# Performance work log

Hardware: AMD Instinct MI355X
Metric: run time of the kernel (lower is better)

Reference implementation:

```python
import jax, jax.numpy as jnp
import numpy as np

B, F, O, DEG = 8192, 512, 512, 15  # degree+1 = 16 basis terms


def setup_inputs() -> dict:
    key = jax.random.key(0)
    k1, k2, k3 = jax.random.split(key, 3)
    x = jax.random.normal(k1, (B, F), dtype=jnp.float32)
    coeffs = jax.random.normal(k2, (F, O, DEG + 1), dtype=jnp.float32) * 0.05
    base_weight = jax.random.normal(k3, (F, O), dtype=jnp.float32) * 0.05
    return {"x": x, "coeffs": coeffs, "base_weight": base_weight}


def _chebyshev_basis(x, degree):
    # x: [B, F] -> basis: [B, F, degree+1], vectorized across all features.
    t = jnp.tanh(x)
    T0 = jnp.ones_like(t)
    T1 = t
    basis = [T0, T1]
    for _ in range(2, degree + 1):
        basis.append(2.0 * t * basis[-1] - basis[-2])
    return jnp.stack(basis, axis=-1)  # [B, F, D+1]


def reference(x, coeffs, base_weight):
    basis = _chebyshev_basis(x, DEG)                      # [B, F, D+1]
    poly_out = jnp.einsum('bin,ion->bo', basis, coeffs)   # [B, O]
    kl = jnp.zeros((1,), dtype=x.dtype)
    residual = x @ base_weight                            # [B, O]
    return (poly_out + residual, kl)
```

## Files before the change

kernel.cpp:

```cpp
#include <hip/hip_runtime.h>
#include <hip/hip_bf16.h>
#include <stdint.h>

#define MB_ 8192
#define FD  512
#define OD  512
#define KD  8704
#define KBASIS 8192
#define BT_KS   1088
#define BT_CHUNKS_PER_CT (BT_KS * 128)
#define BT_BYTES_PER_CT  (BT_CHUNKS_PER_CT * 16)
#define TOFF 65536
#define WS_T    16777216ull
#define WS_XBF  8388608ull
#define WS_BT2  8912896ull
#define WS_P1_OFF (WS_T + WS_XBF + WS_BT2)
#define WS_NEED   (WS_P1_OFF + 16777216ull)

typedef __attribute__((ext_vector_type(4))) float f32x4;
typedef __attribute__((ext_vector_type(8))) short bf16x8;
typedef __attribute__((ext_vector_type(4))) unsigned int u32x4;
typedef __attribute__((ext_vector_type(2))) unsigned int u32x2;

__device__ __forceinline__ void gload_lds16(const void* g, void* l) {
  __builtin_amdgcn_global_load_lds((const __attribute__((address_space(1))) void*)g,
                                   (__attribute__((address_space(3))) void*)l,
                                   16, 0, 0);
}

__device__ __forceinline__ uint32_t bf_rtn(float f) {
  uint32_t u = __float_as_uint(f);
  return (u + 0x7fffu + ((u >> 16) & 1u)) >> 16;
}

__device__ __forceinline__ uint32_t pk(float a, float b) {
  uint32_t r;
  asm("v_cvt_pk_bf16_f32 %0, %1, %2" : "=v"(r) : "v"(a), "v"(b));
  return r;
}

__global__ __launch_bounds__(256) void k_tanh(const float* __restrict__ x,
                                              float* __restrict__ t,
                                              uint16_t* __restrict__ xbf) {
  int i = blockIdx.x * 256 + threadIdx.x;
  f32x4 v = ((const f32x4*)x)[i];
  f32x4 tv;
  tv[0] = tanhf(v[0]); tv[1] = tanhf(v[1]);
  tv[2] = tanhf(v[2]); tv[3] = tanhf(v[3]);
  ((f32x4*)t)[i] = tv;
  u32x2 p;
  p[0] = pk(v[0], v[1]);
  p[1] = pk(v[2], v[3]);
  ((u32x2*)xbf)[i] = p;
}

__global__ __launch_bounds__(256) void k_bt(const float* __restrict__ coeffs,
                                            const float* __restrict__ bw,
                                            uint16_t* __restrict__ bt2,
                                            float* __restrict__ out) {
  int tid = blockIdx.x * 256 + threadIdx.x;
  {
    int o = tid & 511, i = tid >> 9;
    const f32x4* src = (const f32x4*)(coeffs + (((size_t)(i * 512 + o)) << 4));
    f32x4 c0 = src[0], c1 = src[1], c2 = src[2], c3 = src[3];
    u32x4 qa, qb;
    qa[0] = pk(c0[0], c0[1]);
    qa[1] = pk(c0[2], c0[3]);
    qa[2] = pk(c1[0], c1[1]);
    qa[3] = pk(c1[2], c1[3]);
    qb[0] = pk(c2[0], c2[1]);
    qb[1] = pk(c2[2], c2[3]);
    qb[2] = pk(c3[0], c3[1]);
    qb[3] = pk(c3[2], c3[3]);
    int slo = ((i >> 2) << 3) | (i & 3);
    size_t cidx = (size_t)(o >> 7) * BT_CHUNKS_PER_CT + (size_t)slo * 128 + (o & 127);
    u32x4* base = (u32x4*)bt2;
    base[cidx]       = qa;
    base[cidx + 512] = qb;
  }
  {
    int o2 = tid >> 9, i2 = tid & 511;
    size_t cidx = (size_t)(o2 >> 7) * BT_CHUNKS_PER_CT + (size_t)(1024 + (i2 >> 3)) * 128 + (o2 & 127);
    bt2[cidx * 8 + (i2 & 7)] = (uint16_t)bf_rtn(bw[i2 * 512 + o2]);
  }
  if (tid == 0) out[(size_t)MB_ * OD] = 0.0f;
}

template <int MODE>
__device__ __forceinline__ void gemm_body(int bx, char* lds,
                                          const float* __restrict__ t,
                                          const uint16_t* __restrict__ xbf,
                                          const uint16_t* __restrict__ bt2,
                                          float* __restrict__ outp) {
  constexpr int S0 = (MODE == 2) ? 68 : 0;

  const int tid  = threadIdx.x;
  const int lane = tid & 63;
  const int wid  = tid >> 6;
  const int wr   = wid >> 1;
  const int wc   = wid & 1;
  const int l15  = lane & 15, l4 = lane >> 4;

  int idx = bx >> 3;
  int rt  = (bx & 7) * 8 + (idx >> 2);
  int ct  = idx & 3;
  const int brow = rt << 7, bcol = ct << 7;

  const char* btbase = (const char*)bt2 + (size_t)ct * BT_BYTES_PER_CT;
  const int row = brow + wr * 32 + l15;
  const uint16_t* x0 = xbf + (size_t)row * FD;
  const uint16_t* x1 = x0 + (size_t)16 * FD;

  const char* bb0 = lds + l4 * 2048 + (wc * 64 + l15) * 16;
  const char* tb0 = lds + TOFF + (wr * 32 + l15) * 16 + l4 * 4;
  char* sBl = lds + tid * 16;
  char* sTl = lds + TOFF + wid * 1024 + lane * 16;

  const char* sBgBase = btbase + (size_t)tid * 16;
  const char* sTgBase = (const char*)t + (((size_t)(brow + wid * 64 + lane)) * FD) * 4;

  f32x4 acc[2][4];
#pragma unroll
  for (int m = 0; m < 2; ++m)
#pragma unroll
    for (int n = 0; n < 4; ++n) acc[m][n] = (f32x4)0.0f;

  u32x4 pf00 = {}, pf01 = {}, pf10 = {}, pf11 = {};

  auto stageB = [&](int gs, int b2) {
    const char* src = sBgBase + ((size_t)gs << 14);
    gload_lds16(src, sBl + b2 * 16384);
    gload_lds16(src + 8192, sBl + b2 * 16384 + 8192);
  };
  auto stageT = [&](int gs, int b2) {
    if (wid < 2)
      gload_lds16(sTgBase + ((size_t)gs << 4), sTl + b2 * 2048);
  };
  auto chains = [&](const char* tb, u32x4& af00, u32x4& af01,
                    u32x4& af10, u32x4& af11) {
#pragma unroll
    for (int m = 0; m < 2; ++m) {
      float tv = *(const float*)(tb + m * 256);
      float c2 = tv + tv;
      float T0 = 1.0f, T1 = tv;
      float T2  = __builtin_fmaf(c2, T1,  -T0);
      float T3  = __builtin_fmaf(c2, T2,  -T1);
      float T4  = __builtin_fmaf(c2, T3,  -T2);
      float T5  = __builtin_fmaf(c2, T4,  -T3);
      float T6  = __builtin_fmaf(c2, T5,  -T4);
      float T7  = __builtin_fmaf(c2, T6,  -T5);
      float T8  = __builtin_fmaf(c2, T7,  -T6);
      float T9  = __builtin_fmaf(c2, T8,  -T7);
      float T10 = __builtin_fmaf(c2, T9,  -T8);
      float T11 = __builtin_fmaf(c2, T10, -T9);
      float T12 = __builtin_fmaf(c2, T11, -T10);
      float T13 = __builtin_fmaf(c2, T12, -T11);
      float T14 = __builtin_fmaf(c2, T13, -T12);
      float T15 = __builtin_fmaf(c2, T14, -T13);
      u32x4 lo, hi;
      lo[0] = pk(T0,  T1);  lo[1] = pk(T2,  T3);
      lo[2] = pk(T4,  T5);  lo[3] = pk(T6,  T7);
      hi[0] = pk(T8,  T9);  hi[1] = pk(T10, T11);
      hi[2] = pk(T12, T13); hi[3] = pk(T14, T15);
      if (m == 0) { af00 = lo; af01 = hi; }
      else        { af10 = lo; af11 = hi; }
    }
  };
  auto mfma16 = [&](const char* bb, const u32x4& af00, const u32x4& af01,
                    const u32x4& af10, const u32x4& af11) {
    bf16x8 a00 = *(const bf16x8*)&af00;
    bf16x8 a01 = *(const bf16x8*)&af01;
    bf16x8 a10 = *(const bf16x8*)&af10;
    bf16x8 a11 = *(const bf16x8*)&af11;
#pragma unroll
    for (int n = 0; n < 4; ++n) {
      bf16x8 b0 = *(const bf16x8*)(bb + n * 256);
      bf16x8 b1 = *(const bf16x8*)(bb + 8192 + n * 256);
      acc[0][n] = __builtin_amdgcn_mfma_f32_16x16x32_bf16(a00, b0, acc[0][n], 0, 0, 0);
      acc[1][n] = __builtin_amdgcn_mfma_f32_16x16x32_bf16(a10, b0, acc[1][n], 0, 0, 0);
      acc[0][n] = __builtin_amdgcn_mfma_f32_16x16x32_bf16(a01, b1, acc[0][n], 0, 0, 0);
      acc[1][n] = __builtin_amdgcn_mfma_f32_16x16x32_bf16(a11, b1, acc[1][n], 0, 0, 0);
    }
  };
  auto fence_bar = [&]() {
    if (wid < 2) asm volatile("s_waitcnt vmcnt(6)" ::: "memory");
    else         asm volatile("s_waitcnt vmcnt(4)" ::: "memory");
    __builtin_amdgcn_s_barrier();
    __builtin_amdgcn_sched_barrier(0);
  };
  auto pairbody = [&](int s, int c0, int c1) {
    u32x4 af00, af01, af10, af11;
    chains(tb0 + c0 * 2048, af00, af01, af10, af11);
    __builtin_amdgcn_s_setprio(1);
    mfma16(bb0 + c0 * 16384, af00, af01, af10, af11);
    __builtin_amdgcn_s_setprio(0);
    chains(tb0 + c1 * 2048, af00, af01, af10, af11);
    __builtin_amdgcn_s_setprio(1);
    mfma16(bb0 + c1 * 16384, af00, af01, af10, af11);
    __builtin_amdgcn_s_setprio(0);
    __builtin_amdgcn_s_barrier();
    __builtin_amdgcn_sched_barrier(0);
    stageB(S0 + s + 4, c0); stageT(S0 + s + 4, c0);
    stageB(S0 + s + 5, c1); stageT(S0 + s + 5, c1);
    fence_bar();
  };

  stageB(S0 + 0, 0); stageT(S0 + 0, 0);
  stageB(S0 + 1, 1); stageT(S0 + 1, 1);
  stageB(S0 + 2, 2); stageT(S0 + 2, 2);
  stageB(S0 + 3, 3); stageT(S0 + 3, 3);
  fence_bar();

  if constexpr (MODE == 0) {
    for (int s = 0; s < 120; s += 4) { pairbody(s, 0, 1); pairbody(s + 2, 2, 3); }
    pairbody(120, 0, 1); pairbody(122, 2, 3);
    for (int s = 124; s < 136; ++s) {
      u32x4 af00 = pf00, af01 = pf01, af10 = pf10, af11 = pf11;
      if (s >= 126 && s <= 133) stageB(s + 2, (s + 2) & 3);
      if (s >= 127 && s <= 134) {
        int kres = ((s + 1 - 128) << 6) + l4 * 8;
        pf00 = *(const u32x4*)(x0 + kres);
        pf01 = *(const u32x4*)(x0 + kres + 32);
        pf10 = *(const u32x4*)(x1 + kres);
        pf11 = *(const u32x4*)(x1 + kres + 32);
      }
      if (s < 128) chains(tb0 + (s & 3) * 2048, af00, af01, af10, af11);
      mfma16(bb0 + (s & 3) * 16384, af00, af01, af10, af11);
      __syncthreads();
    }
  } else if constexpr (MODE == 1) {
    for (int s = 0; s < 64; s += 4) { pairbody(s, 0, 1); pairbody(s + 2, 2, 3); }
    for (int s = 64; s < 68; ++s) {
      u32x4 af00, af01, af10, af11;
      chains(tb0 + (s & 3) * 2048, af00, af01, af10, af11);
      mfma16(bb0 + (s & 3) * 16384, af00, af01, af10, af11);
      __syncthreads();
    }
  } else {
    for (int s = 0; s < 56; s += 4) { pairbody(s, 0, 1); pairbody(s + 2, 2, 3); }
    for (int s = 56; s < 68; ++s) {
      u32x4 af00 = pf00, af01 = pf01, af10 = pf10, af11 = pf11;
      if (s >= 58 && s <= 65) stageB(68 + s + 2, (s + 2) & 3);
      if (s >= 59 && s <= 66) {
        int kres = ((s + 1 - 60) << 6) + l4 * 8;
        pf00 = *(const u32x4*)(x0 + kres);
        pf01 = *(const u32x4*)(x0 + kres + 32);
        pf10 = *(const u32x4*)(x1 + kres);
        pf11 = *(const u32x4*)(x1 + kres + 32);
      }
      if (s < 60) chains(tb0 + (s & 3) * 2048, af00, af01, af10, af11);
      mfma16(bb0 + (s & 3) * 16384, af00, af01, af10, af11);
      __syncthreads();
    }
  }

#pragma unroll
  for (int m = 0; m < 2; ++m)
#pragma unroll
    for (int n = 0; n < 4; ++n)
#pragma unroll
      for (int r = 0; r < 4; ++r) {
        int grow = brow + wr * 32 + m * 16 + l4 * 4 + r;
        int gcol = bcol + wc * 64 + n * 16 + l15;
        outp[(size_t)grow * OD + gcol] = acc[m][n][r];
      }
}

__global__ __launch_bounds__(512, 4) void k_gemm_split(const float* __restrict__ t,
                                                       const uint16_t* __restrict__ xbf,
                                                       const uint16_t* __restrict__ bt2,
                                                       float* __restrict__ out,
                                                       float* __restrict__ p1) {
  __shared__ __align__(128) char lds[73728];
  if (blockIdx.x < 256) gemm_body<1>(blockIdx.x,       lds, t, xbf, bt2, out);
  else                  gemm_body<2>(blockIdx.x - 256, lds, t, xbf, bt2, p1);
}

__global__ __launch_bounds__(512, 2) void k_gemm_full(const float* __restrict__ t,
                                                      const uint16_t* __restrict__ xbf,
                                                      const uint16_t* __restrict__ bt2,
                                                      float* __restrict__ out) {
  __shared__ __align__(128) char lds[73728];
  gemm_body<0>(blockIdx.x, lds, t, xbf, bt2, out);
}

__global__ __launch_bounds__(256) void k_add(float* __restrict__ out,
                                             const float* __restrict__ p1) {
  size_t i = (size_t)blockIdx.x * 256 + threadIdx.x;
  f32x4 a = ((const f32x4*)out)[i];
  f32x4 b = ((const f32x4*)p1)[i];
  a[0] += b[0]; a[1] += b[1]; a[2] += b[2]; a[3] += b[3];
  ((f32x4*)out)[i] = a;
}

extern "C" void kernel_launch(void* const* d_in, const int* in_sizes, int n_in,
                              void* d_out, int out_size, void* d_ws, size_t ws_size,
                              hipStream_t stream) {
  const float* x      = (const float*)d_in[0];
  const float* coeffs = (const float*)d_in[1];
  const float* bw     = (const float*)d_in[2];
  float* out = (float*)d_out;
  char* ws = (char*)d_ws;

  float*    t   = (float*)ws;
  uint16_t* xbf = (uint16_t*)(ws + WS_T);
  uint16_t* bt2 = (uint16_t*)(ws + WS_T + WS_XBF);
  float*    p1  = (float*)(ws + WS_P1_OFF);

  k_tanh<<<4096, 256, 0, stream>>>(x, t, xbf);
  k_bt<<<1024, 256, 0, stream>>>(coeffs, bw, bt2, out);
  if (ws_size >= WS_NEED) {
    k_gemm_split<<<512, 512, 0, stream>>>(t, xbf, bt2, out, p1);
    k_add<<<4096, 256, 0, stream>>>(out, p1);
  } else {
    k_gemm_full<<<256, 512, 0, stream>>>(t, xbf, bt2, out);
  }
}
```

Measured before the change: 104.2 us.

## Replace split-K partial buffer and add kernel with atomic accumulation; merge prep kernels

Both split-K halves of the GEMM now atomically add their fp32 results into a zeroed output. This removes the separate partial buffer, the extra add kernel and its 32 MB of traffic. The tanh/bf16 conversion and the coefficient repacking kernels are merged into one launch, and the non-split fallback path is deleted. In exchange it adds a memset of the output plus atomic read-modify-write stores, and the summation order of the two halves is no longer fixed.

```diff
diff --git a/kernel.cpp b/kernel.cpp
--- a/kernel.cpp
+++ b/kernel.cpp
@@ -13,9 +13,6 @@
 #define TOFF 65536
 #define WS_T    16777216ull
 #define WS_XBF  8388608ull
-#define WS_BT2  8912896ull
-#define WS_P1_OFF (WS_T + WS_XBF + WS_BT2)
-#define WS_NEED   (WS_P1_OFF + 16777216ull)
 
 typedef __attribute__((ext_vector_type(4))) float f32x4;
 typedef __attribute__((ext_vector_type(8))) short bf16x8;
@@ -39,51 +36,50 @@
   return r;
 }
 
-__global__ __launch_bounds__(256) void k_tanh(const float* __restrict__ x,
+__global__ __launch_bounds__(256) void k_prep(const float* __restrict__ x,
                                               float* __restrict__ t,
-                                              uint16_t* __restrict__ xbf) {
-  int i = blockIdx.x * 256 + threadIdx.x;
-  f32x4 v = ((const f32x4*)x)[i];
-  f32x4 tv;
-  tv[0] = tanhf(v[0]); tv[1] = tanhf(v[1]);
-  tv[2] = tanhf(v[2]); tv[3] = tanhf(v[3]);
-  ((f32x4*)t)[i] = tv;
-  u32x2 p;
-  p[0] = pk(v[0], v[1]);
-  p[1] = pk(v[2], v[3]);
-  ((u32x2*)xbf)[i] = p;
-}
-
-__global__ __launch_bounds__(256) void k_bt(const float* __restrict__ coeffs,
-                                            const float* __restrict__ bw,
-                                            uint16_t* __restrict__ bt2,
-                                            float* __restrict__ out) {
-  int tid = blockIdx.x * 256 + threadIdx.x;
-  {
-    int o = tid & 511, i = tid >> 9;
-    const f32x4* src = (const f32x4*)(coeffs + (((size_t)(i * 512 + o)) << 4));
-    f32x4 c0 = src[0], c1 = src[1], c2 = src[2], c3 = src[3];
-    u32x4 qa, qb;
-    qa[0] = pk(c0[0], c0[1]);
-    qa[1] = pk(c0[2], c0[3]);
-    qa[2] = pk(c1[0], c1[1]);
-    qa[3] = pk(c1[2], c1[3]);
-    qb[0] = pk(c2[0], c2[1]);
-    qb[1] = pk(c2[2], c2[3]);
-    qb[2] = pk(c3[0], c3[1]);
-    qb[3] = pk(c3[2], c3[3]);
-    int slo = ((i >> 2) << 3) | (i & 3);
-    size_t cidx = (size_t)(o >> 7) * BT_CHUNKS_PER_CT + (size_t)slo * 128 + (o & 127);
-    u32x4* base = (u32x4*)bt2;
-    base[cidx]       = qa;
-    base[cidx + 512] = qb;
+                                              uint16_t* __restrict__ xbf,
+                                              const float* __restrict__ coeffs,
+                                              const float* __restrict__ bw,
+                                              uint16_t* __restrict__ bt2) {
+  if (blockIdx.x < 4096) {
+    int i = blockIdx.x * 256 + threadIdx.x;
+    f32x4 v = ((const f32x4*)x)[i];
+    f32x4 tv;
+    tv[0] = tanhf(v[0]); tv[1] = tanhf(v[1]);
+    tv[2] = tanhf(v[2]); tv[3] = tanhf(v[3]);
+    ((f32x4*)t)[i] = tv;
+    u32x2 p;
+    p[0] = pk(v[0], v[1]);
+    p[1] = pk(v[2], v[3]);
+    ((u32x2*)xbf)[i] = p;
+  } else {
+    int tid = (blockIdx.x - 4096) * 256 + threadIdx.x;
+    {
+      int o = tid & 511, i = tid >> 9;
+      const f32x4* src = (const f32x4*)(coeffs + (((size_t)(i * 512 + o)) << 4));
+      f32x4 c0 = src[0], c1 = src[1], c2 = src[2], c3 = src[3];
+      u32x4 qa, qb;
+      qa[0] = pk(c0[0], c0[1]);
+      qa[1] = pk(c0[2], c0[3]);
+      qa[2] = pk(c1[0], c1[1]);
+      qa[3] = pk(c1[2], c1[3]);
+      qb[0] = pk(c2[0], c2[1]);
+      qb[1] = pk(c2[2], c2[3]);
+      qb[2] = pk(c3[0], c3[1]);
+      qb[3] = pk(c3[2], c3[3]);
+      int slo = ((i >> 2) << 3) | (i & 3);
+      size_t cidx = (size_t)(o >> 7) * BT_CHUNKS_PER_CT + (size_t)slo * 128 + (o & 127);
+      u32x4* base = (u32x4*)bt2;
+      base[cidx]       = qa;
+      base[cidx + 512] = qb;
+    }
+    {
+      int o2 = tid >> 9, i2 = tid & 511;
+      size_t cidx = (size_t)(o2 >> 7) * BT_CHUNKS_PER_CT + (size_t)(1024 + (i2 >> 3)) * 128 + (o2 & 127);
+      bt2[cidx * 8 + (i2 & 7)] = (uint16_t)bf_rtn(bw[i2 * 512 + o2]);
+    }
   }
-  {
-    int o2 = tid >> 9, i2 = tid & 511;
-    size_t cidx = (size_t)(o2 >> 7) * BT_CHUNKS_PER_CT + (size_t)(1024 + (i2 >> 3)) * 128 + (o2 & 127);
-    bt2[cidx * 8 + (i2 & 7)] = (uint16_t)bf_rtn(bw[i2 * 512 + o2]);
-  }
-  if (tid == 0) out[(size_t)MB_ * OD] = 0.0f;
 }
 
 template <int MODE>
@@ -211,24 +207,7 @@
   stageB(S0 + 3, 3); stageT(S0 + 3, 3);
   fence_bar();
 
-  if constexpr (MODE == 0) {
-    for (int s = 0; s < 120; s += 4) { pairbody(s, 0, 1); pairbody(s + 2, 2, 3); }
-    pairbody(120, 0, 1); pairbody(122, 2, 3);
-    for (int s = 124; s < 136; ++s) {
-      u32x4 af00 = pf00, af01 = pf01, af10 = pf10, af11 = pf11;
-      if (s >= 126 && s <= 133) stageB(s + 2, (s + 2) & 3);
-      if (s >= 127 && s <= 134) {
-        int kres = ((s + 1 - 128) << 6) + l4 * 8;
-        pf00 = *(const u32x4*)(x0 + kres);
-        pf01 = *(const u32x4*)(x0 + kres + 32);
-        pf10 = *(const u32x4*)(x1 + kres);
-        pf11 = *(const u32x4*)(x1 + kres + 32);
-      }
-      if (s < 128) chains(tb0 + (s & 3) * 2048, af00, af01, af10, af11);
-      mfma16(bb0 + (s & 3) * 16384, af00, af01, af10, af11);
-      __syncthreads();
-    }
-  } else if constexpr (MODE == 1) {
+  if constexpr (MODE == 1) {
     for (int s = 0; s < 64; s += 4) { pairbody(s, 0, 1); pairbody(s + 2, 2, 3); }
     for (int s = 64; s < 68; ++s) {
       u32x4 af00, af01, af10, af11;
@@ -262,35 +241,18 @@
       for (int r = 0; r < 4; ++r) {
         int grow = brow + wr * 32 + m * 16 + l4 * 4 + r;
         int gcol = bcol + wc * 64 + n * 16 + l15;
-        outp[(size_t)grow * OD + gcol] = acc[m][n][r];
+        __hip_atomic_fetch_add(&outp[(size_t)grow * OD + gcol], acc[m][n][r],
+                               __ATOMIC_RELAXED, __HIP_MEMORY_SCOPE_AGENT);
       }
 }
 
 __global__ __launch_bounds__(512, 4) void k_gemm_split(const float* __restrict__ t,
                                                        const uint16_t* __restrict__ xbf,
                                                        const uint16_t* __restrict__ bt2,
-                                                       float* __restrict__ out,
-                                                       float* __restrict__ p1) {
+                                                       float* __restrict__ out) {
   __shared__ __align__(128) char lds[73728];
   if (blockIdx.x < 256) gemm_body<1>(blockIdx.x,       lds, t, xbf, bt2, out);
-  else                  gemm_body<2>(blockIdx.x - 256, lds, t, xbf, bt2, p1);
-}
-
-__global__ __launch_bounds__(512, 2) void k_gemm_full(const float* __restrict__ t,
-                                                      const uint16_t* __restrict__ xbf,
-                                                      const uint16_t* __restrict__ bt2,
-                                                      float* __restrict__ out) {
-  __shared__ __align__(128) char lds[73728];
-  gemm_body<0>(blockIdx.x, lds, t, xbf, bt2, out);
-}
-
-__global__ __launch_bounds__(256) void k_add(float* __restrict__ out,
-                                             const float* __restrict__ p1) {
-  size_t i = (size_t)blockIdx.x * 256 + threadIdx.x;
-  f32x4 a = ((const f32x4*)out)[i];
-  f32x4 b = ((const f32x4*)p1)[i];
-  a[0] += b[0]; a[1] += b[1]; a[2] += b[2]; a[3] += b[3];
-  ((f32x4*)out)[i] = a;
+  else                  gemm_body<2>(blockIdx.x - 256, lds, t, xbf, bt2, out);
 }
 
 extern "C" void kernel_launch(void* const* d_in, const int* in_sizes, int n_in,
@@ -305,14 +267,8 @@
   float*    t   = (float*)ws;
   uint16_t* xbf = (uint16_t*)(ws + WS_T);
   uint16_t* bt2 = (uint16_t*)(ws + WS_T + WS_XBF);
-  float*    p1  = (float*)(ws + WS_P1_OFF);
-
-  k_tanh<<<4096, 256, 0, stream>>>(x, t, xbf);
-  k_bt<<<1024, 256, 0, stream>>>(coeffs, bw, bt2, out);
-  if (ws_size >= WS_NEED) {
-    k_gemm_split<<<512, 512, 0, stream>>>(t, xbf, bt2, out, p1);
-    k_add<<<4096, 256, 0, stream>>>(out, p1);
-  } else {
-    k_gemm_full<<<256, 512, 0, stream>>>(t, xbf, bt2, out);
-  }
-}
+
+  hipMemsetAsync(d_out, 0, (size_t)out_size * sizeof(float), stream);
+  k_prep<<<5120, 256, 0, stream>>>(x, t, xbf, coeffs, bw, bt2);
+  k_gemm_split<<<512, 512, 0, stream>>>(t, xbf, bt2, out);
+}
```

Result: slower. 117.1 us (+12.4%).
